# Kernel tuning notes

Hardware: AMD Instinct MI355X
Metric: run time of the kernel (lower is better)

## Reference

```python
import jax, jax.numpy as jnp
import numpy as np

B, T, C, L = 256, 512, 256, 64
NEG = -1e30  # log-space 'zero'
BLANK = 0


def setup_inputs() -> dict:
    key = jax.random.key(0)
    k1, k2, k3, k4 = jax.random.split(key, 4)
    logits = jax.random.normal(k1, (B, T, C), dtype=jnp.float32)
    targets = jax.random.randint(k2, (B, L), 1, C)            # labels never equal blank (0)
    input_lengths = jax.random.randint(k3, (B,), T - 100, T + 1)
    target_lengths = jax.random.randint(k4, (B,), L // 2, L + 1)
    return dict(logits=logits, targets=targets,
                input_lengths=input_lengths, target_lengths=target_lengths)


def _ctc_loss(logits, targets, input_lengths, target_lengths):
    Bb, Tt, Cc = logits.shape
    Ll = targets.shape[1]
    S = 2 * Ll + 1  # extended label length (blanks interleaved)

    # fused log_softmax over vocab (original does permute then log_softmax; same math)
    logp = jax.nn.log_softmax(logits, axis=-1)  # [B,T,C]

    # extended target sequence: blank, y1, blank, y2, ..., blank
    ext = jnp.zeros((Bb, S), jnp.int32).at[:, 1::2].set(targets.astype(jnp.int32))
    # gather log-probs of extended labels for every timestep: [B,T,S]
    lp_ext = jnp.take_along_axis(logp, jnp.broadcast_to(ext[:, None, :], (Bb, Tt, S)), axis=2)

    # skip transition s-2 -> s allowed iff ext[s] != blank and ext[s] != ext[s-2]
    skip = jnp.zeros((Bb, S), bool).at[:, 2:].set(
        (ext[:, 2:] != BLANK) & (ext[:, 2:] != ext[:, :-2]))

    # alpha at t=0
    alpha0 = (jnp.full((Bb, S), NEG, dtype=logits.dtype)
              .at[:, 0].set(lp_ext[:, 0, 0])
              .at[:, 1].set(lp_ext[:, 0, 1]))

    neg1 = jnp.full((Bb, 1), NEG, dtype=logits.dtype)
    neg2 = jnp.full((Bb, 2), NEG, dtype=logits.dtype)

    def step(alpha, inputs):
        lp_t, t = inputs  # lp_t: [B,S]
        a1 = alpha
        a2 = jnp.concatenate([neg1, alpha[:, :-1]], axis=1)
        a3 = jnp.where(skip, jnp.concatenate([neg2, alpha[:, :-2]], axis=1), NEG)
        new = jnp.logaddexp(jnp.logaddexp(a1, a2), a3) + lp_t
        new = jnp.maximum(new, NEG)  # keep impossible paths bounded
        # freeze alpha for batch rows whose input sequence already ended
        alpha = jnp.where((t < input_lengths)[:, None], new, alpha)
        return alpha, None

    ts = jnp.arange(1, Tt)
    alphaT, _ = jax.lax.scan(step, alpha0, (jnp.swapaxes(lp_ext, 0, 1)[1:], ts))

    tl = target_lengths.astype(jnp.int32)
    a_last = jnp.take_along_axis(alphaT, (2 * tl)[:, None], axis=1)[:, 0]
    a_prev = jnp.take_along_axis(alphaT, (2 * tl - 1)[:, None], axis=1)[:, 0]
    loss = -jnp.logaddexp(a_last, a_prev)            # [B]
    loss = jnp.where(loss > 1e20, 0.0, loss)          # zero_infinity=True
    # reduction='mean': per-sample loss divided by target length, then batch mean
    return (loss / tl.astype(loss.dtype)).mean()


def reference(logits, targets, input_lengths, target_lengths):
    return _ctc_loss(logits, targets, input_lengths, target_lengths)
```

## Files before the change

kernel.cpp:

```cpp
#include <hip/hip_runtime.h>

#define B_ 256
#define T_ 512
#define C_ 256
#define L_ 64
#define S_ 129
#define TCH 64
#define NEG -1e30f
#define LOG2E 1.44269504f
#define LN2 0.69314718f

__device__ __forceinline__ unsigned short f2h(float f) {
    _Float16 h = (_Float16)f;
    return __builtin_bit_cast(unsigned short, h);
}
__device__ __forceinline__ float h2f(unsigned short u) {
    return (float)__builtin_bit_cast(_Float16, u);
}

__device__ __forceinline__ float shr1(float x, float fill) {
    int r = __builtin_amdgcn_update_dpp(__builtin_bit_cast(int, fill),
                                        __builtin_bit_cast(int, x),
                                        0x138, 0xF, 0xF, false);
    return __builtin_bit_cast(float, r);
}

__device__ __forceinline__ float wave_sum(float x) {
#define DPPADD(ctrl)                                                          \
    {                                                                         \
        int _t = __builtin_amdgcn_update_dpp(0, __builtin_bit_cast(int, x),   \
                                             (ctrl), 0xF, 0xF, true);         \
        x += __builtin_bit_cast(float, _t);                                   \
    }
    DPPADD(0x111)
    DPPADD(0x112)
    DPPADD(0x114)
    DPPADD(0x118)
    DPPADD(0x142)
    DPPADD(0x143)
#undef DPPADD
    return __builtin_bit_cast(float,
        __builtin_amdgcn_readlane(__builtin_bit_cast(int, x), 63));
}

__device__ __forceinline__ void ctc_step(float& a0, float& a1, float& a2,
                                         unsigned int q, bool skip) {
    const float lpb = h2f((unsigned short)(q & 0xffffu));
    const float lpo = h2f((unsigned short)(q >> 16));
    const float p = shr1(a1, NEG);
    const float m0 = fmaxf(a0, p), n0 = fminf(a0, p);
    const float a0n = m0 + __log2f(1.0f + exp2f(n0 - m0)) + lpb;
    const float c  = skip ? p : NEG;
    const float m1 = fmaxf(fmaxf(a1, a0), c);
    const float s1 = exp2f(a1 - m1) + exp2f(a0 - m1) + exp2f(c - m1);
    const float a1n = m1 + __log2f(s1) + lpo;
    const float m2 = fmaxf(a2, a1), n2 = fminf(a2, a1);
    const float a2n = m2 + __log2f(1.0f + exp2f(n2 - m2)) + lpb;
    a0 = a0n; a1 = a1n; a2 = a2n;
}

__global__ __launch_bounds__(576) void k_fused(const float* __restrict__ logits,
                                               const int* __restrict__ targets,
                                               const int* __restrict__ in_len,
                                               const int* __restrict__ tg_len,
                                               float* __restrict__ out) {
    const int b = blockIdx.x;
    const int w = threadIdx.x >> 6;
    const int l = threadIdx.x & 63;

    __shared__ unsigned int Gs[2][TCH][64];
    __shared__ int   tgt_sh[L_];
    __shared__ float alpha_sh[S_];

    if (threadIdx.x < L_) tgt_sh[threadIdx.x] = targets[(b << 6) + threadIdx.x];
    __syncthreads();

    const int len = in_len[b];
    float a0 = NEG, a1 = NEG, a2 = NEG;
    bool skip = false;
    if (w == 0) {
        const int tc = tgt_sh[l];
        const int tp = __shfl_up(tc, 1);
        skip = (l >= 1) && (tc != tp);
        __builtin_amdgcn_s_setprio(1);
    }
    const int mytgt = tgt_sh[l];

    const size_t rowbase = (size_t)b * T_;

    for (int k = 0; k < 9; ++k) {
        if (w > 0 && k < 8) {
            const int tt0 = (w - 1) * 8;
            float4 v[8];
            float  lv[8];
            #pragma unroll
            for (int r = 0; r < 8; ++r) {
                const int t = k * TCH + tt0 + r;
                v[r]  = ((const float4*)logits)[(rowbase + t) * 64 + l];
                lv[r] = logits[(rowbase + t) * C_ + mytgt];
            }
            #pragma unroll
            for (int r = 0; r < 8; ++r) {
                const int tt = tt0 + r;
                const float yx = v[r].x * LOG2E, yy = v[r].y * LOG2E;
                const float yz = v[r].z * LOG2E, yw = v[r].w * LOG2E;
                float s = exp2f(yx) + exp2f(yy) + exp2f(yz) + exp2f(yw);
                const float stot = wave_sum(s);
                const float lse2 = __log2f(stot);
                const float lpb  = __builtin_bit_cast(float,
                    __builtin_amdgcn_readfirstlane(__builtin_bit_cast(int, yx))) - lse2;
                const float lpo  = lv[r] * LOG2E - lse2;
                Gs[k & 1][tt][l] = (unsigned int)f2h(lpb)
                                 | ((unsigned int)f2h(lpo) << 16);
            }
        }
        if (w == 0 && k >= 1) {
            const int kb = (k - 1) & 1;
            const int base = (k - 1) * TCH;
            unsigned int qa[8], qb[8];
            #pragma unroll
            for (int j = 0; j < 8; ++j) qa[j] = Gs[kb][j][l];
            if (base == 0) {
                a0 = (l == 0) ? h2f((unsigned short)(qa[0] & 0xffffu)) : NEG;
                a1 = (l == 0) ? h2f((unsigned short)(qa[0] >> 16))     : NEG;
                a2 = NEG;
            }
            for (int g = 0; g < 8; ++g) {
                if (g < 7) {
                    #pragma unroll
                    for (int j = 0; j < 8; ++j)
                        qb[j] = Gs[kb][(g + 1) * 8 + j][l];
                }
                #pragma unroll
                for (int j = 0; j < 8; ++j) {
                    const int t = base + g * 8 + j;
                    if (t >= 1 && t < len)
                        ctc_step(a0, a1, a2, qa[j], skip);
                }
                if (g < 7) {
                    #pragma unroll
                    for (int j = 0; j < 8; ++j) qa[j] = qb[j];
                }
            }
        }
        __syncthreads();
    }

    if (w == 0) {
        alpha_sh[2 * l]     = a0;
        alpha_sh[2 * l + 1] = a1;
        if (l == 63) alpha_sh[128] = a2;
    }
    __syncthreads();
    if (threadIdx.x == 0) {
        const int tl = tg_len[b];
        const float al = alpha_sh[2 * tl];
        const float ap = alpha_sh[2 * tl - 1];
        const float m  = fmaxf(al, ap);
        float loss = -LN2 * (m + __log2f(exp2f(al - m) + exp2f(ap - m)));
        if (loss > 1e20f) loss = 0.0f;
        atomicAdd(out, loss / (float)tl * (1.0f / (float)B_));
    }
}

extern "C" void kernel_launch(void* const* d_in, const int* in_sizes, int n_in,
                              void* d_out, int out_size, void* d_ws, size_t ws_size,
                              hipStream_t stream) {
    const float* logits  = (const float*)d_in[0];
    const int*   targets = (const int*)d_in[1];
    const int*   in_len  = (const int*)d_in[2];
    const int*   tg_len  = (const int*)d_in[3];
    float*       out     = (float*)d_out;

    hipMemsetAsync(d_out, 0, sizeof(float), stream);
    k_fused<<<B_, 576, 0, stream>>>(logits, targets, in_len, tg_len, out);
}
```

Before: 230.6 us.

## Run CTC alpha recursion in linear-space FP64 with periodic wave-wide rescaling

The serial alpha recursion switches from log-space logaddexp (exp2/log2 per state per step) to linear-space probabilities. It uses double-precision adds and multiplies, and a wave-wide max renormalises the values every 32 timesteps while the exponent offset is tracked. Producer waves now store softmax probabilities as two fp32 LDS arrays instead of packed fp16 log-probs. The goal is to shorten the latency-bound serial dependency chain by removing transcendentals, at the cost of FP64 ops, double-width DPP shifts, extra LDS traffic and some risk of underflow between rescales.

```diff
diff --git a/kernel.cpp b/kernel.cpp
--- a/kernel.cpp
+++ b/kernel.cpp
@@ -6,57 +6,70 @@
 #define L_ 64
 #define S_ 129
 #define TCH 64
-#define NEG -1e30f
 #define LOG2E 1.44269504f
 #define LN2 0.69314718f
 
-__device__ __forceinline__ unsigned short f2h(float f) {
-    _Float16 h = (_Float16)f;
-    return __builtin_bit_cast(unsigned short, h);
-}
-__device__ __forceinline__ float h2f(unsigned short u) {
-    return (float)__builtin_bit_cast(_Float16, u);
-}
-
-__device__ __forceinline__ float shr1(float x, float fill) {
-    int r = __builtin_amdgcn_update_dpp(__builtin_bit_cast(int, fill),
-                                        __builtin_bit_cast(int, x),
-                                        0x138, 0xF, 0xF, false);
-    return __builtin_bit_cast(float, r);
+template <int CTRL>
+__device__ __forceinline__ int dpp_mov_i32(int x) {
+    return __builtin_amdgcn_update_dpp(0, x, CTRL, 0xF, 0xF, true);
+}
+
+__device__ __forceinline__ double shr1d(double x) {
+    int2 u = __builtin_bit_cast(int2, x);
+    u.x = dpp_mov_i32<0x138>(u.x);
+    u.y = dpp_mov_i32<0x138>(u.y);
+    return __builtin_bit_cast(double, u);
+}
+
+template <int CTRL>
+__device__ __forceinline__ double dpp_mov_f64(double x) {
+    int2 u = __builtin_bit_cast(int2, x);
+    u.x = dpp_mov_i32<CTRL>(u.x);
+    u.y = dpp_mov_i32<CTRL>(u.y);
+    return __builtin_bit_cast(double, u);
 }
 
 __device__ __forceinline__ float wave_sum(float x) {
 #define DPPADD(ctrl)                                                          \
-    {                                                                         \
-        int _t = __builtin_amdgcn_update_dpp(0, __builtin_bit_cast(int, x),   \
-                                             (ctrl), 0xF, 0xF, true);         \
-        x += __builtin_bit_cast(float, _t);                                   \
-    }
-    DPPADD(0x111)
-    DPPADD(0x112)
-    DPPADD(0x114)
-    DPPADD(0x118)
-    DPPADD(0x142)
-    DPPADD(0x143)
+    x += __builtin_bit_cast(float, dpp_mov_i32<ctrl>(__builtin_bit_cast(int, x)));
+    DPPADD(0x111) DPPADD(0x112) DPPADD(0x114)
+    DPPADD(0x118) DPPADD(0x142) DPPADD(0x143)
 #undef DPPADD
     return __builtin_bit_cast(float,
         __builtin_amdgcn_readlane(__builtin_bit_cast(int, x), 63));
 }
 
-__device__ __forceinline__ void ctc_step(float& a0, float& a1, float& a2,
-                                         unsigned int q, bool skip) {
-    const float lpb = h2f((unsigned short)(q & 0xffffu));
-    const float lpo = h2f((unsigned short)(q >> 16));
-    const float p = shr1(a1, NEG);
-    const float m0 = fmaxf(a0, p), n0 = fminf(a0, p);
-    const float a0n = m0 + __log2f(1.0f + exp2f(n0 - m0)) + lpb;
-    const float c  = skip ? p : NEG;
-    const float m1 = fmaxf(fmaxf(a1, a0), c);
-    const float s1 = exp2f(a1 - m1) + exp2f(a0 - m1) + exp2f(c - m1);
-    const float a1n = m1 + __log2f(s1) + lpo;
-    const float m2 = fmaxf(a2, a1), n2 = fminf(a2, a1);
-    const float a2n = m2 + __log2f(1.0f + exp2f(n2 - m2)) + lpb;
-    a0 = a0n; a1 = a1n; a2 = a2n;
+__device__ __forceinline__ double wave_max_d(double x) {
+    x = fmax(x, dpp_mov_f64<0x111>(x));
+    x = fmax(x, dpp_mov_f64<0x112>(x));
+    x = fmax(x, dpp_mov_f64<0x114>(x));
+    x = fmax(x, dpp_mov_f64<0x118>(x));
+    x = fmax(x, dpp_mov_f64<0x142>(x));
+    x = fmax(x, dpp_mov_f64<0x143>(x));
+    int2 u = __builtin_bit_cast(int2, x);
+    u.x = __builtin_amdgcn_readlane(u.x, 63);
+    u.y = __builtin_amdgcn_readlane(u.y, 63);
+    return __builtin_bit_cast(double, u);
+}
+
+__device__ __forceinline__ void rescale(double& a0, double& a1, double& a2, int& e) {
+    const double m = wave_max_d(fmax(fmax(a0, a1), a2));
+    const int hi = __builtin_bit_cast(int2, m).y;
+    int ex = ((hi >> 20) & 0x7ff) - 1023;
+    if (m == 0.0) ex = 0;
+    e += ex;
+    int2 fb; fb.x = 0; fb.y = (1023 - ex) << 20;
+    const double f = __builtin_bit_cast(double, fb);
+    a0 *= f; a1 *= f; a2 *= f;
+}
+
+__device__ __forceinline__ float log2_pos(double a) {
+    if (a == 0.0) return -1e30f;
+    int2 u = __builtin_bit_cast(int2, a);
+    const int ex = ((u.y >> 20) & 0x7ff) - 1023;
+    u.y = (u.y & 0x800FFFFF) | (1023 << 20);
+    const float mf = (float)__builtin_bit_cast(double, u);
+    return __log2f(mf) + (float)ex;
 }
 
 __global__ __launch_bounds__(576) void k_fused(const float* __restrict__ logits,
@@ -68,7 +81,8 @@
     const int w = threadIdx.x >> 6;
     const int l = threadIdx.x & 63;
 
-    __shared__ unsigned int Gs[2][TCH][64];
+    __shared__ float Pb[2][TCH][64];
+    __shared__ float Po[2][TCH][64];
     __shared__ int   tgt_sh[L_];
     __shared__ float alpha_sh[S_];
 
@@ -76,7 +90,8 @@
     __syncthreads();
 
     const int len = in_len[b];
-    float a0 = NEG, a1 = NEG, a2 = NEG;
+    double a0 = 0.0, a1 = 0.0, a2 = 0.0;
+    int scale_total = 0;
     bool skip = false;
     if (w == 0) {
         const int tc = tgt_sh[l];
@@ -102,44 +117,53 @@
             #pragma unroll
             for (int r = 0; r < 8; ++r) {
                 const int tt = tt0 + r;
-                const float yx = v[r].x * LOG2E, yy = v[r].y * LOG2E;
-                const float yz = v[r].z * LOG2E, yw = v[r].w * LOG2E;
-                float s = exp2f(yx) + exp2f(yy) + exp2f(yz) + exp2f(yw);
-                const float stot = wave_sum(s);
-                const float lse2 = __log2f(stot);
-                const float lpb  = __builtin_bit_cast(float,
-                    __builtin_amdgcn_readfirstlane(__builtin_bit_cast(int, yx))) - lse2;
-                const float lpo  = lv[r] * LOG2E - lse2;
-                Gs[k & 1][tt][l] = (unsigned int)f2h(lpb)
-                                 | ((unsigned int)f2h(lpo) << 16);
+                const float e0 = exp2f(v[r].x * LOG2E);
+                const float e1 = exp2f(v[r].y * LOG2E);
+                const float e2 = exp2f(v[r].z * LOG2E);
+                const float e3 = exp2f(v[r].w * LOG2E);
+                const float stot = wave_sum(e0 + e1 + e2 + e3);
+                const float rs = __builtin_amdgcn_rcpf(stot);
+                const float eb = __builtin_bit_cast(float,
+                    __builtin_amdgcn_readfirstlane(__builtin_bit_cast(int, e0)));
+                Pb[k & 1][tt][l] = eb * rs;
+                Po[k & 1][tt][l] = exp2f(lv[r] * LOG2E) * rs;
             }
         }
         if (w == 0 && k >= 1) {
             const int kb = (k - 1) & 1;
             const int base = (k - 1) * TCH;
-            unsigned int qa[8], qb[8];
+            float pba[8], poa[8], pbb[8], pob[8];
             #pragma unroll
-            for (int j = 0; j < 8; ++j) qa[j] = Gs[kb][j][l];
+            for (int j = 0; j < 8; ++j) { pba[j] = Pb[kb][j][l]; poa[j] = Po[kb][j][l]; }
             if (base == 0) {
-                a0 = (l == 0) ? h2f((unsigned short)(qa[0] & 0xffffu)) : NEG;
-                a1 = (l == 0) ? h2f((unsigned short)(qa[0] >> 16))     : NEG;
-                a2 = NEG;
+                a0 = (l == 0) ? (double)pba[0] : 0.0;
+                a1 = (l == 0) ? (double)poa[0] : 0.0;
+                a2 = 0.0;
             }
             for (int g = 0; g < 8; ++g) {
                 if (g < 7) {
                     #pragma unroll
-                    for (int j = 0; j < 8; ++j)
-                        qb[j] = Gs[kb][(g + 1) * 8 + j][l];
+                    for (int j = 0; j < 8; ++j) {
+                        pbb[j] = Pb[kb][(g + 1) * 8 + j][l];
+                        pob[j] = Po[kb][(g + 1) * 8 + j][l];
+                    }
                 }
                 #pragma unroll
                 for (int j = 0; j < 8; ++j) {
                     const int t = base + g * 8 + j;
-                    if (t >= 1 && t < len)
-                        ctc_step(a0, a1, a2, qa[j], skip);
+                    if (t >= 1 && t < len) {
+                        const double p = shr1d(a1);
+                        const double c = skip ? p : 0.0;
+                        const double a0n = (a0 + p) * (double)pba[j];
+                        const double a1n = ((a1 + a0) + c) * (double)poa[j];
+                        const double a2n = (a2 + a1) * (double)pba[j];
+                        a0 = a0n; a1 = a1n; a2 = a2n;
+                    }
                 }
+                if (g == 3 || g == 7) rescale(a0, a1, a2, scale_total);
                 if (g < 7) {
                     #pragma unroll
-                    for (int j = 0; j < 8; ++j) qa[j] = qb[j];
+                    for (int j = 0; j < 8; ++j) { pba[j] = pbb[j]; poa[j] = pob[j]; }
                 }
             }
         }
@@ -147,9 +171,9 @@
     }
 
     if (w == 0) {
-        alpha_sh[2 * l]     = a0;
-        alpha_sh[2 * l + 1] = a1;
-        if (l == 63) alpha_sh[128] = a2;
+        alpha_sh[2 * l]     = log2_pos(a0);
+        alpha_sh[2 * l + 1] = log2_pos(a1);
+        if (l == 63) alpha_sh[128] = log2_pos(a2);
     }
     __syncthreads();
     if (threadIdx.x == 0) {
@@ -157,8 +181,9 @@
         const float al = alpha_sh[2 * tl];
         const float ap = alpha_sh[2 * tl - 1];
         const float m  = fmaxf(al, ap);
-        float loss = -LN2 * (m + __log2f(exp2f(al - m) + exp2f(ap - m)));
-        if (loss > 1e20f) loss = 0.0f;
+        const float lse2 = m + __log2f(exp2f(al - m) + exp2f(ap - m));
+        float loss = -LN2 * (lse2 + (float)scale_total);
+        if (!(loss < 1e20f)) loss = 0.0f;
         atomicAdd(out, loss / (float)tl * (1.0f / (float)B_));
     }
 }
@@ -172,6 +197,6 @@
     const int*   tg_len  = (const int*)d_in[3];
     float*       out     = (float*)d_out;
 
-    hipMemsetAsync(d_out, 0, sizeof(float), stream);
+    (void)hipMemsetAsync(d_out, 0, sizeof(float), stream);
     k_fused<<<B_, 576, 0, stream>>>(logits, targets, in_len, tg_len, out);
 }
```

New measurement: 204.2 us. 1.13x faster.
